# Performance work log

Measured on AMD Instinct MI355X. Metric: run time of the kernel, lower is better.

Reference implementation:

```python
import jax, jax.numpy as jnp
import numpy as np

B, N, C, H = 8, 1025, 768, 12
HD = C // H  # 64
SCALE = HD ** -0.5


def rotate_half(x):
    x1, x2 = jnp.split(x, 2, axis=-1)
    return jnp.concatenate((-x2, x1), axis=-1)


def apply_rope(x, sin, cos):
    return x * cos + rotate_half(x) * sin


def setup_inputs() -> dict:
    key = jax.random.key(0)
    ks = jax.random.split(key, 7)
    x = jax.random.normal(ks[0], (B, N, C), dtype=jnp.float32)
    sin = jax.random.normal(ks[1], (N - 1, HD), dtype=jnp.float32)
    cos = jax.random.normal(ks[2], (N - 1, HD), dtype=jnp.float32)
    s = 1.0 / np.sqrt(C)
    qkv_w = jax.random.normal(ks[3], (3 * C, C), dtype=jnp.float32) * s
    qkv_b = jnp.zeros((3 * C,), dtype=jnp.float32)
    proj_w = jax.random.normal(ks[4], (C, C), dtype=jnp.float32) * s
    proj_b = jnp.zeros((C,), dtype=jnp.float32)
    return {"x": x, "sin": sin, "cos": cos, "qkv_w": qkv_w, "qkv_b": qkv_b,
            "proj_w": proj_w, "proj_b": proj_b}


def reference(x, sin, cos, qkv_w, qkv_b, proj_w, proj_b):
    b, n, c = x.shape
    qkv = x @ qkv_w.T + qkv_b                      # [B,N,3C]
    qkv = qkv.reshape(b, n, 3, H, HD)
    qkv = jnp.transpose(qkv, (2, 0, 3, 1, 4))      # [3,B,H,N,HD]
    q, k, v = qkv[0], qkv[1], qkv[2]
    # RoPE on patch tokens only (cls token at index 0 excluded)
    q_patch = apply_rope(q[:, :, 1:, :], sin, cos)
    k_patch = apply_rope(k[:, :, 1:, :], sin, cos)
    q = jnp.concatenate((q[:, :, :1, :], q_patch), axis=2)
    k = jnp.concatenate((k[:, :, :1, :], k_patch), axis=2)
    attn = jnp.einsum('bhqd,bhkd->bhqk', q, k) * SCALE
    attn = jax.nn.softmax(attn, axis=-1)
    out = jnp.einsum('bhqk,bhkd->bhqd', attn, v)   # [B,H,N,HD]
    out = jnp.transpose(out, (0, 2, 1, 3)).reshape(b, n, c)
    out = out @ proj_w.T + proj_b
    return out
```

## Files before the change

kernel.cpp:

```cpp
#include <hip/hip_runtime.h>
#include <hip/hip_bf16.h>

constexpr int NTOK   = 1025;
constexpr int M      = 8 * NTOK;
constexpr int MP     = 8320;
constexpr int KDIM   = 768;
constexpr int NQKV   = 2304;
constexpr int NKVPAD = 1088;
constexpr float SCALEL2 = 0.125f * 1.44269504f;

using bf16x8 = __attribute__((ext_vector_type(8))) short;
using f32x4  = __attribute__((ext_vector_type(4))) float;

__device__ __forceinline__ f32x4 mfma_bf16(bf16x8 a, bf16x8 b, f32x4 c) {
  return __builtin_amdgcn_mfma_f32_16x16x32_bf16(a, b, c, 0, 0, 0);
}

__device__ __forceinline__ void gl16(const void* g, void* l) {
  __builtin_amdgcn_global_load_lds(
      (const __attribute__((address_space(1))) void*)g,
      (__attribute__((address_space(3))) void*)l, 16, 0, 0);
}

__device__ __forceinline__ float exp2_raw(float x) {
  float r;
  asm("v_exp_f32 %0, %1" : "=v"(r) : "v"(x));
  return r;
}
__device__ __forceinline__ __hip_bfloat16 cvt_bf16_raw(float x) {
  unsigned u;
  asm("v_cvt_pk_bf16_f32 %0, %1, %2" : "=v"(u) : "v"(x), "v"(x));
  union { unsigned short s; __hip_bfloat16 b; } c;
  c.s = (unsigned short)(u & 0xffffu);
  return c.b;
}

constexpr size_t SZ_X     = (size_t)MP * KDIM * 2;
constexpr size_t SZ_WQ    = (size_t)NQKV * KDIM * 2;
constexpr size_t SZ_PW    = (size_t)KDIM * KDIM * 2;
constexpr size_t SZ_QK    = (size_t)96 * NTOK * 64 * 2;
constexpr size_t SZ_VT    = (size_t)96 * 64 * NKVPAD * 2;
constexpr size_t OFF_XHI  = 0;
constexpr size_t OFF_XLO  = OFF_XHI + SZ_X;
constexpr size_t OFF_WQHI = OFF_XLO + SZ_X;
constexpr size_t OFF_PWHI = OFF_WQHI + SZ_WQ;
constexpr size_t OFF_PWLO = OFF_PWHI + SZ_PW;
constexpr size_t OFF_Q    = OFF_PWLO + SZ_PW;
constexpr size_t OFF_K    = OFF_Q + SZ_QK;
constexpr size_t OFF_VT   = OFF_K + SZ_QK;
constexpr size_t OFF_AO   = OFF_VT + SZ_VT;

__global__ void k_split(const float* __restrict__ src, __hip_bfloat16* __restrict__ hi,
                        __hip_bfloat16* __restrict__ lo, int n_src, int n_dst) {
  int i = blockIdx.x * 256 + threadIdx.x;
  if (i >= n_dst) return;
  float v = (i < n_src) ? src[i] : 0.0f;
  __hip_bfloat16 h = __float2bfloat16(v);
  hi[i] = h;
  lo[i] = __float2bfloat16(v - __bfloat162float(h));
}

__global__ void k_tobf16(const float* __restrict__ src, __hip_bfloat16* __restrict__ dst,
                         int n_src, int n_dst) {
  int i = blockIdx.x * 256 + threadIdx.x;
  if (i >= n_dst) return;
  dst[i] = __float2bfloat16((i < n_src) ? src[i] : 0.0f);
}

__global__ void k_zero_vt(__hip_bfloat16* __restrict__ vt) {
  int i = blockIdx.x * 256 + threadIdx.x;
  constexpr int NPADC = NKVPAD - NTOK;
  if (i >= 96 * 64 * NPADC) return;
  int r = i / NPADC;
  int c = NTOK + (i - r * NPADC);
  vt[(size_t)r * NKVPAD + c] = __float2bfloat16(0.0f);
}

template <int EPI, int NT, int NBX>
__global__ __launch_bounds__(256) void k_gemm(
    const __hip_bfloat16* __restrict__ Ahi, const __hip_bfloat16* __restrict__ Asec,
    const __hip_bfloat16* __restrict__ Bhi, const float* __restrict__ bias,
    const float* __restrict__ sinp, const float* __restrict__ cosp,
    __hip_bfloat16* __restrict__ o_q, __hip_bfloat16* __restrict__ o_k,
    __hip_bfloat16* __restrict__ o_vt, float* __restrict__ o_f32) {
  const int tid = threadIdx.x;
  const int w = tid >> 6, lane = tid & 63;
  const int wm = w >> 1, wn = w & 1;
  const int l15 = lane & 15, q4 = lane >> 4;

  const int nwg = gridDim.x;
  const int orig = blockIdx.x;
  const int qc = nwg >> 3, rc = nwg & 7;
  const int xcd = orig & 7, o8 = orig >> 3;
  const int wg =
      (xcd < rc ? xcd * (qc + 1) : rc * (qc + 1) + (xcd - rc) * qc) + o8;
  const int bx = wg % NBX, by = wg / NBX;
  const int mBase = by * 128, nBase = bx * 128;

  __shared__ __hip_bfloat16 sm[2][NT * 4096];
  constexpr int OFFB = (NT - 1) * 8192;

  const char* p0 = (const char*)Ahi + (size_t)mBase * (KDIM * 2);
  const char* p1 = (const char*)Asec + (size_t)nBase * (KDIM * 2);
  const char* p2 = (const char*)Bhi + (size_t)nBase * (KDIM * 2);

  const int slog = ((tid & 3) ^ ((tid >> 3) & 3)) << 4;
  const int ph = ((q4 ^ ((l15 >> 1) & 3)) << 4);

  auto stage = [&](int kt, int buf) {
    const int kofs = kt * 64;
    char* base = (char*)sm[buf];
#pragma unroll
    for (int i = 0; i < 2; ++i) {
      const int c = i * 256 + tid;
      const size_t rb = (size_t)(i * 64 + (tid >> 2)) * (KDIM * 2) + slog + kofs;
      gl16(p0 + rb, base + (size_t)c * 16);
      if (NT == 3) gl16(p1 + rb, base + 8192 + (size_t)c * 16);
      gl16(p2 + rb, base + OFFB + (size_t)c * 16);
    }
  };

  f32x4 acc[4][4] = {};

  stage(0, 0);
  __syncthreads();

  constexpr int NKT = KDIM / 32;
  for (int kt = 0; kt < NKT; ++kt) {
    const int cur = kt & 1;
    if (kt + 1 < NKT) stage(kt + 1, cur ^ 1);
    char* s0 = (char*)sm[cur];
    char* s1 = s0 + 8192;
    char* s2 = s0 + OFFB;
    bf16x8 a0[4], b0[4], b1[4];
#pragma unroll
    for (int mt = 0; mt < 4; ++mt) {
      const int r = wm * 64 + mt * 16 + l15;
      a0[mt] = *(const bf16x8*)(s0 + r * 64 + ph);
    }
#pragma unroll
    for (int nt = 0; nt < 4; ++nt) {
      const int r = wn * 64 + nt * 16 + l15;
      b0[nt] = *(const bf16x8*)(s2 + r * 64 + ph);
      if (NT == 3) b1[nt] = *(const bf16x8*)(s1 + r * 64 + ph);
    }
    __builtin_amdgcn_s_setprio(1);
#pragma unroll
    for (int mt = 0; mt < 4; ++mt)
#pragma unroll
      for (int nt = 0; nt < 4; ++nt) {
        acc[mt][nt] = mfma_bf16(a0[mt], b0[nt], acc[mt][nt]);
        if (NT == 3) acc[mt][nt] = mfma_bf16(a0[mt], b1[nt], acc[mt][nt]);
      }
    __builtin_amdgcn_s_setprio(0);
    __syncthreads();
  }

#pragma unroll
  for (int mt = 0; mt < 4; ++mt)
#pragma unroll
    for (int j = 0; j < 4; ++j) {
      const int gm = mBase + wm * 64 + mt * 16 + q4 * 4 + j;
      if (gm >= M) continue;
      if (EPI == 0) {
        const int b = gm / NTOK;
        const int t = gm - b * NTOK;
#pragma unroll
        for (int nt = 0; nt < 4; ++nt) {
          const int gc = nBase + wn * 64 + nt * 16 + l15;
          float v = acc[mt][nt][j] + bias[gc];
          const int three = gc / 768;
          const int hd = gc - three * 768;
          const int h = hd >> 6, d = hd & 63;
          const int bh = b * 12 + h;
          if (three == 2) {
            o_vt[((size_t)bh * 64 + d) * NKVPAD + t] = __float2bfloat16(v);
          } else {
            if (t > 0) {
              const float pv = acc[mt][nt ^ 2][j] + bias[gc ^ 32];
              const int so = (t - 1) * 64 + d;
              v = v * cosp[so] + ((d < 32) ? -pv : pv) * sinp[so];
            }
            if (three == 0)
              o_q[((size_t)bh * NTOK + t) * 64 + d] = __float2bfloat16(v);
            else
              o_k[((size_t)bh * NTOK + t) * 64 + d] = __float2bfloat16(v * SCALEL2);
          }
        }
      } else {
#pragma unroll
        for (int nt = 0; nt < 4; ++nt) {
          const int gc = nBase + wn * 64 + nt * 16 + l15;
          o_f32[(size_t)gm * 768 + gc] = acc[mt][nt][j] + bias[gc];
        }
      }
    }
}

__global__ __launch_bounds__(256) void k_attn(
    const __hip_bfloat16* __restrict__ Q, const __hip_bfloat16* __restrict__ Kk,
    const __hip_bfloat16* __restrict__ VT, __hip_bfloat16* __restrict__ ao) {
  __shared__ __hip_bfloat16 Kt[2][64 * 64];
  __shared__ __hip_bfloat16 Vt[2][64 * 64];
  __shared__ __hip_bfloat16 Pl[4][32][72];
  const int tid = threadIdx.x, w = tid >> 6, lane = tid & 63;
  const int l15 = lane & 15, q4 = lane >> 4;
  const int id = blockIdx.x;
  const int xcd = id & 7, sub = id >> 3;
  const int hh = sub / 9;
  const int bh = xcd * 12 + hh;
  const int qb = (sub - hh * 9) * 128 + w * 32;
  const size_t qbase = (size_t)bh * NTOK * 64;
  const char* Kb = (const char*)(Kk + qbase);
  const char* Vb = (const char*)(VT + (size_t)bh * 64 * NKVPAD);

  int frag_off[2][4];
#pragma unroll
  for (int f = 0; f < 4; ++f) {
    const int row = f * 16 + l15;
#pragma unroll
    for (int ks = 0; ks < 2; ++ks)
      frag_off[ks][f] = row * 128 + (((ks * 4 + q4) ^ (row & 7)) << 4);
  }
  int stRow[2], sch16[2], stK[2], stV[2], ldsOff[2];
#pragma unroll
  for (int i = 0; i < 2; ++i) {
    const int c = i * 256 + tid;
    const int row = c >> 3;
    stRow[i] = row;
    sch16[i] = ((c & 7) ^ (row & 7)) << 4;
    stK[i] = row * 128 + sch16[i];
    stV[i] = row * (NKVPAD * 2) + sch16[i];
    ldsOff[i] = c * 16;
  }
  int pw_off[2][4], pa_off[2][2];
#pragma unroll
  for (int mt = 0; mt < 2; ++mt) {
#pragma unroll
    for (int j = 0; j < 4; ++j)
      pw_off[mt][j] = ((w * 32 + mt * 16 + q4 * 4 + j) * 72 + l15) * 2;
#pragma unroll
    for (int ks = 0; ks < 2; ++ks)
      pa_off[mt][ks] = ((w * 32 + mt * 16 + l15) * 72 + ks * 32 + q4 * 8) * 2;
  }
  char* Plc = (char*)&Pl[0][0][0];

  bf16x8 qa[2][2];
#pragma unroll
  for (int mt = 0; mt < 2; ++mt) {
    int t = qb + mt * 16 + l15;
    if (t > NTOK - 1) t = NTOK - 1;
#pragma unroll
    for (int ks = 0; ks < 2; ++ks)
      qa[mt][ks] = *(const bf16x8*)(Q + qbase + (size_t)t * 64 + ks * 32 + q4 * 8);
  }

  f32x4 accO[2][4] = {};
  float mrun[2][4], lpart[2][4];
#pragma unroll
  for (int mt = 0; mt < 2; ++mt)
#pragma unroll
    for (int j = 0; j < 4; ++j) {
      mrun[mt][j] = -1e30f;
      lpart[mt][j] = 0.0f;
    }

  auto stageKV = [&](int kt, int b) {
    const int kb0 = kt * 64;
#pragma unroll
    for (int i = 0; i < 2; ++i) {
      const char* srcK;
      if (kt == 16) {
        const int srow = min(kb0 + stRow[i], NTOK - 1);
        srcK = Kb + (size_t)srow * 128 + sch16[i];
      } else {
        srcK = Kb + (size_t)kb0 * 128 + stK[i];
      }
      gl16(srcK, (char*)&Kt[b][0] + ldsOff[i]);
      gl16(Vb + (size_t)kb0 * 2 + stV[i], (char*)&Vt[b][0] + ldsOff[i]);
    }
  };

  auto step = [&](int kt, int cur, bool last) {
    f32x4 s[2][4] = {};
    {
      const char* Kc = (const char*)&Kt[cur][0];
      bf16x8 kfr[2][4];
#pragma unroll
      for (int nt = 0; nt < 4; ++nt)
#pragma unroll
        for (int ks = 0; ks < 2; ++ks)
          kfr[ks][nt] = *(const bf16x8*)(Kc + frag_off[ks][nt]);
      __builtin_amdgcn_s_setprio(1);
#pragma unroll
      for (int mt = 0; mt < 2; ++mt)
#pragma unroll
        for (int nt = 0; nt < 4; ++nt)
#pragma unroll
          for (int ks = 0; ks < 2; ++ks)
            s[mt][nt] = mfma_bf16(qa[mt][ks], kfr[ks][nt], s[mt][nt]);
      __builtin_amdgcn_s_setprio(0);
    }
    if (last) {
#pragma unroll
      for (int nt = 0; nt < 4; ++nt)
        if (1024 + nt * 16 + l15 > NTOK - 1) {
#pragma unroll
          for (int mt = 0; mt < 2; ++mt)
#pragma unroll
            for (int j = 0; j < 4; ++j) s[mt][nt][j] = -1e30f;
        }
    }
    float smax[2][4];
    bool okl = true;
#pragma unroll
    for (int mt = 0; mt < 2; ++mt)
#pragma unroll
      for (int j = 0; j < 4; ++j) {
        const float a =
            fmaxf(fmaxf(s[mt][0][j], s[mt][1][j]), fmaxf(s[mt][2][j], s[mt][3][j]));
        smax[mt][j] = a;
        okl = okl && (a <= mrun[mt][j] + 8.0f);
      }
    if (!__all((int)okl)) {
#pragma unroll
      for (int mt = 0; mt < 2; ++mt)
#pragma unroll
        for (int j = 0; j < 4; ++j) {
          float m0 = smax[mt][j];
#pragma unroll
          for (int off = 1; off < 16; off <<= 1) m0 = fmaxf(m0, __shfl_xor(m0, off));
          const float mnew = fmaxf(mrun[mt][j], m0);
          const float fsc = exp2_raw(mrun[mt][j] - mnew);
          lpart[mt][j] *= fsc;
          mrun[mt][j] = mnew;
#pragma unroll
          for (int nd = 0; nd < 4; ++nd) accO[mt][nd][j] *= fsc;
        }
    }
#pragma unroll
    for (int mt = 0; mt < 2; ++mt)
#pragma unroll
      for (int j = 0; j < 4; ++j) {
        float acc = 0.0f;
        char* pw = Plc + pw_off[mt][j];
#pragma unroll
        for (int nt = 0; nt < 4; ++nt) {
          const float p = exp2_raw(s[mt][nt][j] - mrun[mt][j]);
          acc += p;
          *(__hip_bfloat16*)(pw + nt * 32) = cvt_bf16_raw(p);
        }
        lpart[mt][j] += acc;
      }
    bf16x8 pa[2][2], vf[2][4];
#pragma unroll
    for (int mt = 0; mt < 2; ++mt)
#pragma unroll
      for (int ks = 0; ks < 2; ++ks)
        pa[mt][ks] = *(const bf16x8*)(Plc + pa_off[mt][ks]);
    {
      const char* Vc = (const char*)&Vt[cur][0];
#pragma unroll
      for (int nd = 0; nd < 4; ++nd)
#pragma unroll
        for (int ks = 0; ks < 2; ++ks)
          vf[ks][nd] = *(const bf16x8*)(Vc + frag_off[ks][nd]);
    }
    __builtin_amdgcn_s_setprio(1);
#pragma unroll
    for (int mt = 0; mt < 2; ++mt)
#pragma unroll
      for (int nd = 0; nd < 4; ++nd)
#pragma unroll
        for (int ks = 0; ks < 2; ++ks)
          accO[mt][nd] = mfma_bf16(pa[mt][ks], vf[ks][nd], accO[mt][nd]);
    __builtin_amdgcn_s_setprio(0);
  };

  stageKV(0, 0);
  __syncthreads();
  for (int kt = 0; kt < 17; ++kt) {
    const int cur = kt & 1;
    if (kt < 16) stageKV(kt + 1, cur ^ 1);
    step(kt, cur, kt == 16);
    __syncthreads();
  }

  const int b = bh / 12, h = bh - (bh / 12) * 12;
#pragma unroll
  for (int mt = 0; mt < 2; ++mt)
#pragma unroll
    for (int j = 0; j < 4; ++j) {
      float sum = lpart[mt][j];
#pragma unroll
      for (int off2 = 1; off2 < 16; off2 <<= 1) sum += __shfl_xor(sum, off2);
      const int t = qb + mt * 16 + q4 * 4 + j;
      if (t > NTOK - 1) continue;
      const float inv = 1.0f / sum;
      const size_t ro = ((size_t)(b * NTOK + t)) * 768 + h * 64;
#pragma unroll
      for (int nd = 0; nd < 4; ++nd) {
        const int d = nd * 16 + l15;
        ao[ro + d] = __float2bfloat16(accO[mt][nd][j] * inv);
      }
    }
}

extern "C" void kernel_launch(void* const* d_in, const int* in_sizes, int n_in,
                              void* d_out, int out_size, void* d_ws, size_t ws_size,
                              hipStream_t stream) {
  const float* x = (const float*)d_in[0];
  const float* sinp = (const float*)d_in[1];
  const float* cosp = (const float*)d_in[2];
  const float* qkvw = (const float*)d_in[3];
  const float* qkvb = (const float*)d_in[4];
  const float* projw = (const float*)d_in[5];
  const float* projb = (const float*)d_in[6];

  char* ws = (char*)d_ws;
  __hip_bfloat16* xhi = (__hip_bfloat16*)(ws + OFF_XHI);
  __hip_bfloat16* wqhi = (__hip_bfloat16*)(ws + OFF_WQHI);
  __hip_bfloat16* pwhi = (__hip_bfloat16*)(ws + OFF_PWHI);
  __hip_bfloat16* pwlo = (__hip_bfloat16*)(ws + OFF_PWLO);
  __hip_bfloat16* qb = (__hip_bfloat16*)(ws + OFF_Q);
  __hip_bfloat16* kb = (__hip_bfloat16*)(ws + OFF_K);
  __hip_bfloat16* vt = (__hip_bfloat16*)(ws + OFF_VT);
  __hip_bfloat16* ao = (__hip_bfloat16*)(ws + OFF_AO);

  {
    int n_src = M * KDIM, n_dst = MP * KDIM;
    k_tobf16<<<(n_dst + 255) / 256, 256, 0, stream>>>(x, xhi, n_src, n_dst);
    int nw = NQKV * KDIM;
    k_tobf16<<<(nw + 255) / 256, 256, 0, stream>>>(qkvw, wqhi, nw, nw);
    int np = KDIM * KDIM;
    k_split<<<(np + 255) / 256, 256, 0, stream>>>(projw, pwhi, pwlo, np, np);
    int nz = 96 * 64 * (NKVPAD - NTOK);
    k_zero_vt<<<(nz + 255) / 256, 256, 0, stream>>>(vt);
  }
  k_gemm<0, 2, 18><<<dim3(18 * 65), 256, 0, stream>>>(
      xhi, xhi, wqhi, qkvb, sinp, cosp, qb, kb, vt, nullptr);
  k_attn<<<dim3(864), 256, 0, stream>>>(qb, kb, vt, ao);
  k_gemm<1, 3, 6><<<dim3(6 * 65), 256, 0, stream>>>(
      ao, pwlo, pwhi, projb, nullptr, nullptr, nullptr, nullptr, nullptr,
      (float*)d_out);
}
```

Baseline: 224.8 us.

## Triple-buffer GEMM and attention LDS staging with vmcnt-based waits

Switches both the GEMM and attention kernels from double- to triple-buffered LDS tiles, prefetching two tiles ahead. Each iteration now waits with a partial s_waitcnt vmcnt and a single barrier instead of a full __syncthreads at both ends. The aim is to hide global-to-LDS load latency better and remove one barrier per iteration. It raises LDS use, which may lower occupancy, and correctness depends on the hand-picked vmcnt values matching the number of outstanding loads per stage.

```diff
diff --git a/kernel.cpp b/kernel.cpp
--- a/kernel.cpp
+++ b/kernel.cpp
@@ -20,6 +20,15 @@
   __builtin_amdgcn_global_load_lds(
       (const __attribute__((address_space(1))) void*)g,
       (__attribute__((address_space(3))) void*)l, 16, 0, 0);
+}
+
+template <int N> __device__ __forceinline__ void wait_vmcnt() {
+  if constexpr (N == 0)
+    asm volatile("s_waitcnt vmcnt(0)" ::: "memory");
+  else if constexpr (N == 4)
+    asm volatile("s_waitcnt vmcnt(4)" ::: "memory");
+  else if constexpr (N == 6)
+    asm volatile("s_waitcnt vmcnt(6)" ::: "memory");
 }
 
 __device__ __forceinline__ float exp2_raw(float x) {
@@ -97,7 +106,7 @@
   const int bx = wg % NBX, by = wg / NBX;
   const int mBase = by * 128, nBase = bx * 128;
 
-  __shared__ __hip_bfloat16 sm[2][NT * 4096];
+  __shared__ __hip_bfloat16 sm[3][NT * 4096];
   constexpr int OFFB = (NT - 1) * 8192;
 
   const char* p0 = (const char*)Ahi + (size_t)mBase * (KDIM * 2);
@@ -123,13 +132,17 @@
   f32x4 acc[4][4] = {};
 
   stage(0, 0);
-  __syncthreads();
+  stage(1, 1);
 
   constexpr int NKT = KDIM / 32;
   for (int kt = 0; kt < NKT; ++kt) {
-    const int cur = kt & 1;
-    if (kt + 1 < NKT) stage(kt + 1, cur ^ 1);
-    char* s0 = (char*)sm[cur];
+    if (kt < NKT - 1)
+      wait_vmcnt<2 * NT>();
+    else
+      wait_vmcnt<0>();
+    __builtin_amdgcn_s_barrier();
+    if (kt + 2 < NKT) stage(kt + 2, (kt + 2) % 3);
+    char* s0 = (char*)sm[kt % 3];
     char* s1 = s0 + 8192;
     char* s2 = s0 + OFFB;
     bf16x8 a0[4], b0[4], b1[4];
@@ -153,7 +166,6 @@
         if (NT == 3) acc[mt][nt] = mfma_bf16(a0[mt], b1[nt], acc[mt][nt]);
       }
     __builtin_amdgcn_s_setprio(0);
-    __syncthreads();
   }
 
 #pragma unroll
@@ -200,8 +212,8 @@
 __global__ __launch_bounds__(256) void k_attn(
     const __hip_bfloat16* __restrict__ Q, const __hip_bfloat16* __restrict__ Kk,
     const __hip_bfloat16* __restrict__ VT, __hip_bfloat16* __restrict__ ao) {
-  __shared__ __hip_bfloat16 Kt[2][64 * 64];
-  __shared__ __hip_bfloat16 Vt[2][64 * 64];
+  __shared__ __hip_bfloat16 Kt[3][64 * 64];
+  __shared__ __hip_bfloat16 Vt[3][64 * 64];
   __shared__ __hip_bfloat16 Pl[4][32][72];
   const int tid = threadIdx.x, w = tid >> 6, lane = tid & 63;
   const int l15 = lane & 15, q4 = lane >> 4;
@@ -378,12 +390,15 @@
   };
 
   stageKV(0, 0);
-  __syncthreads();
+  stageKV(1, 1);
   for (int kt = 0; kt < 17; ++kt) {
-    const int cur = kt & 1;
-    if (kt < 16) stageKV(kt + 1, cur ^ 1);
-    step(kt, cur, kt == 16);
-    __syncthreads();
+    if (kt < 16)
+      wait_vmcnt<4>();
+    else
+      wait_vmcnt<0>();
+    __builtin_amdgcn_s_barrier();
+    if (kt + 2 < 17) stageKV(kt + 2, (kt + 2) % 3);
+    step(kt, kt % 3, kt == 16);
   }
 
   const int b = bh / 12, h = bh - (bh / 12) * 12;
```

Measured after the change: 223.0 us. Within noise of the previous version (-0.8%).
